# Optimization experiments

Measured on AMD Instinct MI355X. Metric: run time of the kernel, lower is better.

## Reference

```python
import jax, jax.numpy as jnp
import numpy as np

HEADS = 8
DIM_HEAD = 64
NUM_LANDMARKS = 256
PINV_ITERS = 6
SCALE = DIM_HEAD ** -0.5
KERNEL = 33
PAD = KERNEL // 2


def moore_penrose_iter_pinv(x, iters=PINV_ITERS):
    # x: [b, h, m, m]
    abs_x = jnp.abs(x)
    col = abs_x.sum(axis=-1)
    row = abs_x.sum(axis=-2)
    # global max over all batch/head entries, as in the torch code
    z = jnp.swapaxes(x, -1, -2) / (jnp.max(col) * jnp.max(row))
    I = jnp.eye(x.shape[-1], dtype=x.dtype)
    for _ in range(iters):
        xz = x @ z
        z = 0.25 * z @ (13.0 * I - xz @ (15.0 * I - xz @ (7.0 * I - xz)))
    return z


def setup_inputs() -> dict:
    key = jax.random.key(0)
    k1, k2, k3, k4 = jax.random.split(key, 4)
    b, n, dim = 4, 4096, 512
    inner = HEADS * DIM_HEAD
    return {
        "x": jax.random.normal(k1, (b, n, dim), dtype=jnp.float32),
        "w_qkv": jax.random.normal(k2, (dim, 3 * inner), dtype=jnp.float32) * 0.02,
        "w_out": jax.random.normal(k3, (inner, dim), dtype=jnp.float32) * 0.02,
        "b_out": jnp.zeros((dim,), dtype=jnp.float32),
        "conv_w": jax.random.normal(k4, (HEADS, 1, KERNEL, 1), dtype=jnp.float32) * 0.1,
    }


def reference(x, w_qkv, w_out, b_out, conv_w):
    b, n, dim = x.shape
    h, m = HEADS, NUM_LANDMARKS
    # n is a multiple of m, so the original's left-padding branch is a no-op
    qkv = x @ w_qkv  # [b, n, 3*h*d]
    q, k, v = jnp.split(qkv, 3, axis=-1)

    def split_heads(t):
        return t.reshape(b, n, h, DIM_HEAD).transpose(0, 2, 1, 3)  # [b,h,n,d]

    q, k, v = split_heads(q), split_heads(k), split_heads(v)
    q = q * SCALE

    l = n // m  # landmark group size
    q_l = q.reshape(b, h, m, l, DIM_HEAD).mean(axis=3)  # [b,h,m,d]
    k_l = k.reshape(b, h, m, l, DIM_HEAD).mean(axis=3)

    sim1 = jnp.einsum("bhid,bhjd->bhij", q, k_l)   # [b,h,n,m]
    sim2 = jnp.einsum("bhid,bhjd->bhij", q_l, k_l)  # [b,h,m,m]
    sim3 = jnp.einsum("bhid,bhjd->bhij", q_l, k)   # [b,h,m,n]

    attn1 = jax.nn.softmax(sim1, axis=-1)
    attn2 = jax.nn.softmax(sim2, axis=-1)
    attn3 = jax.nn.softmax(sim3, axis=-1)

    attn2_inv = moore_penrose_iter_pinv(attn2, PINV_ITERS)
    out = attn1 @ (attn2_inv @ (attn3 @ v))  # [b,h,n,d]

    # residual depthwise conv along sequence dim (kernel 33x1, groups=heads)
    res = jax.lax.conv_general_dilated(
        v, conv_w,
        window_strides=(1, 1),
        padding=((PAD, PAD), (0, 0)),
        dimension_numbers=("NCHW", "OIHW", "NCHW"),
        feature_group_count=h,
    )
    out = out + res

    out = out.transpose(0, 2, 1, 3).reshape(b, n, h * DIM_HEAD)
    out = out @ w_out + b_out
    return out  # out[:, -n:] is identity since no padding was applied
```

## Files before the change

kernel.cpp:

```cpp
#include <hip/hip_runtime.h>
#include <math.h>


#define QKV_STRIDE 262144
#define LM_STRIDE 16384
#define MM_STRIDE 65536

typedef float f32x4 __attribute__((ext_vector_type(4)));
typedef short bf8 __attribute__((ext_vector_type(8)));
typedef short s4v __attribute__((ext_vector_type(4)));

__device__ __forceinline__ unsigned short f2bf_(float f) {
  unsigned u = __float_as_uint(f);
  u += 0x7FFFu + ((u >> 16) & 1u);
  return (unsigned short)(u >> 16);
}
__device__ __forceinline__ float bf2f_(unsigned short h) {
  return __uint_as_float(((unsigned)h) << 16);
}
__device__ __forceinline__ bf8 pack8(const float4 a, const float4 b) {
  bf8 r;
  r[0] = (short)f2bf_(a.x); r[1] = (short)f2bf_(a.y);
  r[2] = (short)f2bf_(a.z); r[3] = (short)f2bf_(a.w);
  r[4] = (short)f2bf_(b.x); r[5] = (short)f2bf_(b.y);
  r[6] = (short)f2bf_(b.z); r[7] = (short)f2bf_(b.w);
  return r;
}

__global__ __launch_bounds__(256) void zero_scal(float* scal) {
  if (threadIdx.x < 2) scal[threadIdx.x] = 0.0f;
}

__global__ __launch_bounds__(256) void transpose_bf16(const float* __restrict__ src,
                                                      short* __restrict__ dst,
                                                      int R, int C) {
  __shared__ float T[32][33];
  const int t = threadIdx.x;
  const int c0 = blockIdx.x * 32, r0 = blockIdx.y * 32;
  const int tr = t >> 3, tc = (t & 7) << 2;
  float4 vsrc = *(const float4*)&src[(size_t)(r0 + tr) * C + c0 + tc];
  T[tr][tc + 0] = vsrc.x; T[tr][tc + 1] = vsrc.y;
  T[tr][tc + 2] = vsrc.z; T[tr][tc + 3] = vsrc.w;
  __syncthreads();
  s4v o;
  o[0] = (short)f2bf_(T[tc + 0][tr]);
  o[1] = (short)f2bf_(T[tc + 1][tr]);
  o[2] = (short)f2bf_(T[tc + 2][tr]);
  o[3] = (short)f2bf_(T[tc + 3][tr]);
  *(s4v*)&dst[(size_t)(c0 + tr) * R + r0 + tc] = o;
}

__global__ __launch_bounds__(256) void gemm_qkv_mfma(const float* __restrict__ x,
                                                     const short* __restrict__ wT,
                                                     short* __restrict__ qb16,
                                                     short* __restrict__ kb16,
                                                     short* __restrict__ vT16) {
  __shared__ short SMEM[17408];
  short* As = SMEM;
  short* Bs = SMEM + 4096;
  const int tid = threadIdx.x;
  const int lane = tid & 63, w = tid >> 6;
  const int wr = w >> 1, wc = w & 1;
  const int bid = (blockIdx.x & 7) * 192 + (blockIdx.x >> 3);
  const int bn = bid % 12, bm = bid / 12;
  const int gm0 = bm * 128, gn0 = bn * 128;
  const int mA0 = (tid >> 6) * 16 + (tid & 15), kA0 = ((tid >> 4) & 3) * 8;
  const int s1 = tid + 256;
  const int mA1 = (s1 >> 6) * 16 + (s1 & 15), kA1 = ((s1 >> 4) & 3) * 8;
  f32x4 acc[4][4];
#pragma unroll
  for (int i = 0; i < 4; ++i)
#pragma unroll
    for (int j = 0; j < 4; ++j) acc[i][j] = (f32x4){0.f, 0.f, 0.f, 0.f};
  for (int kt = 0; kt < 16; ++kt) {
    const int k0 = kt * 32;
    float4 a0 = *(const float4*)&x[(size_t)(gm0 + mA0) * 512 + k0 + kA0];
    float4 a1 = *(const float4*)&x[(size_t)(gm0 + mA0) * 512 + k0 + kA0 + 4];
    float4 a2 = *(const float4*)&x[(size_t)(gm0 + mA1) * 512 + k0 + kA1];
    float4 a3 = *(const float4*)&x[(size_t)(gm0 + mA1) * 512 + k0 + kA1 + 4];
    bf8 b0 = *(const bf8*)&wT[(size_t)(gn0 + mA0) * 512 + k0 + kA0];
    bf8 b1 = *(const bf8*)&wT[(size_t)(gn0 + mA1) * 512 + k0 + kA1];
    __syncthreads();
    *(bf8*)&As[tid * 8] = pack8(a0, a1);
    *(bf8*)&As[s1 * 8] = pack8(a2, a3);
    *(bf8*)&Bs[tid * 8] = b0;
    *(bf8*)&Bs[s1 * 8] = b1;
    __syncthreads();
    bf8 af[4], bf[4];
#pragma unroll
    for (int i = 0; i < 4; ++i) {
      af[i] = *(const bf8*)&As[((wr * 4 + i) * 64 + lane) * 8];
      bf[i] = *(const bf8*)&Bs[((wc * 4 + i) * 64 + lane) * 8];
    }
#pragma unroll
    for (int i = 0; i < 4; ++i)
#pragma unroll
      for (int j = 0; j < 4; ++j)
        acc[i][j] = __builtin_amdgcn_mfma_f32_16x16x32_bf16(af[i], bf[j], acc[i][j], 0, 0, 0);
  }
  const int which = bn >> 2;
  const int qd = lane >> 4, c = lane & 15;
  if (which < 2) {
    short* dst = which == 0 ? qb16 : kb16;
    const float scale = which == 0 ? 0.125f : 1.0f;
#pragma unroll
    for (int i = 0; i < 4; ++i)
#pragma unroll
      for (int j = 0; j < 4; ++j) {
        const int col = gn0 + wc * 64 + j * 16 + c;
        const int head = (col >> 6) & 7, dd = col & 63;
#pragma unroll
        for (int r = 0; r < 4; ++r) {
          const int row = gm0 + wr * 64 + i * 16 + qd * 4 + r;
          const int b = row >> 12, seq = row & 4095;
          dst[(size_t)(b * 8 + head) * QKV_STRIDE + seq * 64 + dd] =
              (short)f2bf_(acc[i][j][r] * scale);
        }
      }
  } else {
    __syncthreads();
#pragma unroll
    for (int i = 0; i < 4; ++i)
#pragma unroll
      for (int j = 0; j < 4; ++j) {
        const int colL = wc * 64 + j * 16 + c;
#pragma unroll
        for (int r = 0; r < 4; ++r) {
          const int rowL = wr * 64 + i * 16 + qd * 4 + r;
          SMEM[colL * 136 + rowL] = (short)f2bf_(acc[i][j][r]);
        }
      }
    __syncthreads();
    const int b = gm0 >> 12, seq0 = gm0 & 4095;
    const int dcol = tid >> 1, half = tid & 1;
    const int col = gn0 + dcol;
    const int head = (col >> 6) & 7, d = col & 63;
    const short* src = &SMEM[dcol * 136 + half * 64];
    short* dstp = &vT16[(size_t)(b * 8 + head) * QKV_STRIDE + (size_t)d * 4096 +
                        seq0 + half * 64];
#pragma unroll
    for (int u = 0; u < 16; ++u) *(s4v*)&dstp[u * 4] = *(const s4v*)&src[u * 4];
  }
}

__global__ __launch_bounds__(256) void lmk_mean(const short* __restrict__ qb16,
                                                const short* __restrict__ kb16,
                                                float* __restrict__ ql,
                                                float* __restrict__ kl,
                                                short* __restrict__ klb16) {
  const int g = blockIdx.x * 256 + threadIdx.x;
  const int dd = g & 63, mi = (g >> 6) & 255, bh = g >> 14;
  const size_t base = (size_t)bh * QKV_STRIDE + mi * 1024 + dd;
  float sq = 0.f, sk = 0.f;
#pragma unroll
  for (int jj = 0; jj < 16; ++jj) {
    sq += bf2f_((unsigned short)qb16[base + jj * 64]);
    sk += bf2f_((unsigned short)kb16[base + jj * 64]);
  }
  const float qv = sq * 0.0625f, kv = sk * 0.0625f;
  ql[g] = qv;
  kl[g] = kv;
  klb16[g] = (short)f2bf_(kv);
}

__global__ __launch_bounds__(256) void sim2_softmax(const float* __restrict__ ql,
                                                    const float* __restrict__ kl,
                                                    float* __restrict__ x2) {
  const int blk = blockIdx.x;
  const int bh = blk >> 4, rg = blk & 15;
  __shared__ float Qs[16][64];
  __shared__ float Ks[64][68];
  __shared__ float S[16][257];
  __shared__ float red[16][17];
  __shared__ float rowinv[16];
  const int tid = threadIdx.x;
  const int r = tid >> 4, jc = tid & 15;
#pragma unroll
  for (int u = 0; u < 4; ++u) {
    int t2 = tid + u * 256;
    Qs[t2 >> 6][t2 & 63] =
        ql[(size_t)bh * LM_STRIDE + (rg * 16 + (t2 >> 6)) * 64 + (t2 & 63)];
  }
  for (int c = 0; c < 4; ++c) {
    __syncthreads();
#pragma unroll
    for (int u = 0; u < 4; ++u) {
      int t4 = tid + u * 256;
      int row = t4 >> 4, c4 = (t4 & 15) << 2;
      *(float4*)&Ks[row][c4] =
          *(const float4*)&kl[(size_t)bh * LM_STRIDE + (c * 64 + row) * 64 + c4];
    }
    __syncthreads();
#pragma unroll
    for (int s = 0; s < 4; ++s) {
      const int jj = jc + (s << 4);
      float acc = 0.f;
#pragma unroll
      for (int k4 = 0; k4 < 16; ++k4) {
        const float4 a = *(const float4*)&Qs[r][k4 << 2];
        const float4 bb = *(const float4*)&Ks[jj][k4 << 2];
        acc += a.x * bb.x + a.y * bb.y + a.z * bb.z + a.w * bb.w;
      }
      S[r][(c << 6) + jj] = acc;
    }
  }
  __syncthreads();
  float pm = -3.0e38f;
#pragma unroll
  for (int u = 0; u < 16; ++u) pm = fmaxf(pm, S[r][jc + (u << 4)]);
  red[r][jc] = pm;
  __syncthreads();
  float m = red[r][0];
#pragma unroll
  for (int u = 1; u < 16; ++u) m = fmaxf(m, red[r][u]);
  __syncthreads();
  float ps = 0.f;
#pragma unroll
  for (int u = 0; u < 16; ++u) {
    const int j = jc + (u << 4);
    const float e = __expf(S[r][j] - m);
    S[r][j] = e;
    ps += e;
  }
  red[r][jc] = ps;
  __syncthreads();
  if (jc == 0) {
    float sum = 0.f;
#pragma unroll
    for (int u = 0; u < 16; ++u) sum += red[r][u];
    rowinv[r] = 1.0f / sum;
  }
  __syncthreads();
  for (int idx = tid; idx < 4096; idx += 256) {
    const int rr = idx >> 8, j = idx & 255;
    x2[(size_t)bh * MM_STRIDE + (rg * 16 + rr) * 256 + j] = S[rr][j] * rowinv[rr];
  }
}

__global__ __launch_bounds__(256) void colrow_max(const float* __restrict__ x2,
                                                  float* __restrict__ scal) {
  const int bh = blockIdx.x;
  const int tid = threadIdx.x;
  const float* xb = x2 + (size_t)bh * MM_STRIDE;
  float cs = 0.f, rs = 0.f;
  for (int j = 0; j < 256; ++j) cs += fabsf(xb[tid * 256 + j]);
  for (int i = 0; i < 256; ++i) rs += fabsf(xb[i * 256 + tid]);
  __shared__ float rc[256], rr[256];
  rc[tid] = cs; rr[tid] = rs;
  __syncthreads();
  for (int st = 128; st > 0; st >>= 1) {
    if (tid < st) {
      rc[tid] = fmaxf(rc[tid], rc[tid + st]);
      rr[tid] = fmaxf(rr[tid], rr[tid + st]);
    }
    __syncthreads();
  }
  if (tid == 0) {
    atomicMax((int*)&scal[0], __float_as_int(rc[0]));
    atomicMax((int*)&scal[1], __float_as_int(rr[0]));
  }
}

__global__ __launch_bounds__(256) void tscale2(const float* __restrict__ x2,
                                               const float* __restrict__ scal,
                                               float* __restrict__ z0,
                                               float* __restrict__ z0t) {
  const int g = blockIdx.x * 256 + threadIdx.x;
  const int j = g & 255, i = (g >> 8) & 255, bh = g >> 16;
  const float inv = 1.0f / (scal[0] * scal[1]);
  const float val = x2[g] * inv;
  z0t[g] = val;
  z0[(size_t)bh * MM_STRIDE + j * 256 + i] = val;
}

__global__ __launch_bounds__(256) void pinv_mfma(const float* __restrict__ A,
                                                 const float* __restrict__ BT,
                                                 const float* __restrict__ E,
                                                 float* __restrict__ C,
                                                 float* __restrict__ CT,
                                                 float alpha, float beta,
                                                 int wantC, int wantT) {
  __shared__ short Ahi[2048], Alo[2048], Bhi[2048], Blo[2048];
  __shared__ float Tbuf[64 * 68];
  const int tid = threadIdx.x;
  const int lane = tid & 63, w = tid >> 6;
  const int bid = blockIdx.x;
  const int xcd = bid & 7, y = bid >> 3;
  const int t16 = y & 15, bgrp = y >> 4;
  const int batch = bgrp * 8 + xcd;
  const int tm = t16 >> 2, tn = t16 & 3;
  const float* Ab = A + (size_t)batch * MM_STRIDE;
  const float* BTb = BT + (size_t)batch * MM_STRIDE;
  const float* Eb = E + (size_t)batch * MM_STRIDE;
  const int ml = (tid >> 6) * 16 + (tid & 15), koff = ((tid >> 4) & 3) * 8;
  f32x4 acc[4];
#pragma unroll
  for (int j = 0; j < 4; ++j) acc[j] = (f32x4){0.f, 0.f, 0.f, 0.f};
  for (int kt = 0; kt < 8; ++kt) {
    const int k0 = kt * 32;
    float4 a0 = *(const float4*)&Ab[(size_t)(tm * 64 + ml) * 256 + k0 + koff];
    float4 a1 = *(const float4*)&Ab[(size_t)(tm * 64 + ml) * 256 + k0 + koff + 4];
    float4 b0 = *(const float4*)&BTb[(size_t)(tn * 64 + ml) * 256 + k0 + koff];
    float4 b1 = *(const float4*)&BTb[(size_t)(tn * 64 + ml) * 256 + k0 + koff + 4];
    __syncthreads();
    {
      bf8 hi, lo;
      const float fa[8] = {a0.x, a0.y, a0.z, a0.w, a1.x, a1.y, a1.z, a1.w};
#pragma unroll
      for (int e = 0; e < 8; ++e) {
        unsigned short h = f2bf_(fa[e]);
        hi[e] = (short)h;
        lo[e] = (short)f2bf_(fa[e] - bf2f_(h));
      }
      *(bf8*)&Ahi[tid * 8] = hi;
      *(bf8*)&Alo[tid * 8] = lo;
      const float fb[8] = {b0.x, b0.y, b0.z, b0.w, b1.x, b1.y, b1.z, b1.w};
#pragma unroll
      for (int e = 0; e < 8; ++e) {
        unsigned short h = f2bf_(fb[e]);
        hi[e] = (short)h;
        lo[e] = (short)f2bf_(fb[e] - bf2f_(h));
      }
      *(bf8*)&Bhi[tid * 8] = hi;
      *(bf8*)&Blo[tid * 8] = lo;
    }
    __syncthreads();
    bf8 ah = *(const bf8*)&Ahi[(w * 64 + lane) * 8];
    bf8 al = *(const bf8*)&Alo[(w * 64 + lane) * 8];
#pragma unroll
    for (int j = 0; j < 4; ++j) {
      bf8 bh = *(const bf8*)&Bhi[(j * 64 + lane) * 8];
      bf8 bl = *(const bf8*)&Blo[(j * 64 + lane) * 8];
      acc[j] = __builtin_amdgcn_mfma_f32_16x16x32_bf16(ah, bh, acc[j], 0, 0, 0);
      acc[j] = __builtin_amdgcn_mfma_f32_16x16x32_bf16(ah, bl, acc[j], 0, 0, 0);
      acc[j] = __builtin_amdgcn_mfma_f32_16x16x32_bf16(al, bh, acc[j], 0, 0, 0);
    }
  }
  float* Cb = C + (size_t)batch * MM_STRIDE;
  float* CTb = CT + (size_t)batch * MM_STRIDE;
  const int qd = lane >> 4, c = lane & 15;
  float vals[4][4];
#pragma unroll
  for (int j = 0; j < 4; ++j) {
    const int col = tn * 64 + j * 16 + c;
#pragma unroll
    for (int r = 0; r < 4; ++r) {
      const int row = tm * 64 + w * 16 + qd * 4 + r;
      vals[j][r] = alpha * Eb[(size_t)row * 256 + col] + beta * acc[j][r];
      if (wantC) Cb[(size_t)row * 256 + col] = vals[j][r];
    }
  }
  if (wantT) {
    __syncthreads();
#pragma unroll
    for (int j = 0; j < 4; ++j)
#pragma unroll
      for (int r = 0; r < 4; ++r)
        Tbuf[(j * 16 + c) * 68 + w * 16 + qd * 4 + r] = vals[j][r];
    __syncthreads();
    const int ctr = tid >> 2, seg = (tid & 3) * 16;
#pragma unroll
    for (int u = 0; u < 4; ++u) {
      float4 o = *(const float4*)&Tbuf[ctr * 68 + seg + u * 4];
      *(float4*)&CTb[(size_t)(tn * 64 + ctr) * 256 + tm * 64 + seg + u * 4] = o;
    }
  }
}

__global__ __launch_bounds__(256) void attn3_flash(const float* __restrict__ ql,
                                                   const short* __restrict__ kb16,
                                                   const short* __restrict__ vT16,
                                                   float* __restrict__ opart,
                                                   float* __restrict__ mpart,
                                                   float* __restrict__ lpart) {
  const int kc = blockIdx.x;
  const int rt = blockIdx.y;
  const int bh = blockIdx.z;
  __shared__ short Pa[4][4096];
  const int tid = threadIdx.x, lane = tid & 63, w = tid >> 6;
  const int qd = lane >> 4, c = lane & 15;
  const int rw = rt * 64 + w * 16;
  const float* qlp = ql + (size_t)bh * LM_STRIDE;
  const short* kp = kb16 + (size_t)bh * QKV_STRIDE;
  const short* vp = vT16 + (size_t)bh * QKV_STRIDE;
  short* Pw = &Pa[w][0];
  bf8 af[2];
#pragma unroll
  for (int st = 0; st < 2; ++st) {
    float4 x0 = *(const float4*)&qlp[(size_t)(rw + c) * 64 + st * 32 + qd * 8];
    float4 x1 = *(const float4*)&qlp[(size_t)(rw + c) * 64 + st * 32 + qd * 8 + 4];
    af[st] = pack8(x0, x1);
  }
  float m[4], l[4];
#pragma unroll
  for (int r = 0; r < 4; ++r) { m[r] = -3.0e38f; l[r] = 0.f; }
  f32x4 accO[4];
#pragma unroll
  for (int nb = 0; nb < 4; ++nb) accO[nb] = (f32x4){0.f, 0.f, 0.f, 0.f};
  for (int it = 0; it < 4; ++it) {
    const int kb0 = kc * 1024 + it * 256;
    f32x4 acc[16];
#pragma unroll
    for (int j = 0; j < 16; ++j) acc[j] = (f32x4){0.f, 0.f, 0.f, 0.f};
#pragma unroll
    for (int st = 0; st < 2; ++st)
#pragma unroll
      for (int j = 0; j < 16; ++j) {
        bf8 bfk = *(const bf8*)&kp[(size_t)(kb0 + j * 16 + c) * 64 + st * 32 + qd * 8];
        acc[j] = __builtin_amdgcn_mfma_f32_16x16x32_bf16(af[st], bfk, acc[j], 0, 0, 0);
      }
#pragma unroll
    for (int r = 0; r < 4; ++r) {
      float mx = acc[0][r];
#pragma unroll
      for (int j = 1; j < 16; ++j) mx = fmaxf(mx, acc[j][r]);
      mx = fmaxf(mx, __shfl_xor(mx, 1));
      mx = fmaxf(mx, __shfl_xor(mx, 2));
      mx = fmaxf(mx, __shfl_xor(mx, 4));
      mx = fmaxf(mx, __shfl_xor(mx, 8));
      const float mN = fmaxf(m[r], mx);
      const float a = __expf(m[r] - mN);
      m[r] = mN;
      l[r] *= a;
#pragma unroll
      for (int nb = 0; nb < 4; ++nb) accO[nb][r] *= a;
      float s = 0.f;
#pragma unroll
      for (int j = 0; j < 16; ++j) {
        const float e = __expf(acc[j][r] - mN);
        acc[j][r] = e;
        s += e;
      }
      s += __shfl_xor(s, 1);
      s += __shfl_xor(s, 2);
      s += __shfl_xor(s, 4);
      s += __shfl_xor(s, 8);
      l[r] += s;
    }
#pragma unroll
    for (int j = 0; j < 16; ++j) {
      const int kcol = j * 16 + c;
      const int kb8 = kcol >> 5;
      const int la_base = 16 * ((kcol >> 3) & 3);
      const int j8 = kcol & 7;
#pragma unroll
      for (int r = 0; r < 4; ++r) {
        const int rl = qd * 4 + r;
        Pw[(kb8 * 64 + la_base + rl) * 8 + j8] = (short)f2bf_(acc[j][r]);
      }
    }
#pragma unroll
    for (int kbk = 0; kbk < 8; ++kbk) {
      bf8 ap = *(const bf8*)&Pw[(kbk * 64 + lane) * 8];
#pragma unroll
      for (int nb = 0; nb < 4; ++nb) {
        bf8 bv = *(const bf8*)&vp[(size_t)(nb * 16 + c) * 4096 + kb0 + kbk * 32 + qd * 8];
        accO[nb] = __builtin_amdgcn_mfma_f32_16x16x32_bf16(ap, bv, accO[nb], 0, 0, 0);
      }
    }
  }
  const size_t ob = ((size_t)kc * 32 + bh) * 256 + rt * 64;
#pragma unroll
  for (int nb = 0; nb < 4; ++nb)
#pragma unroll
    for (int r = 0; r < 4; ++r)
      opart[(ob + w * 16 + qd * 4 + r) * 64 + nb * 16 + c] = accO[nb][r];
  if (c == 0) {
#pragma unroll
    for (int r = 0; r < 4; ++r) {
      mpart[ob + w * 16 + qd * 4 + r] = m[r];
      lpart[ob + w * 16 + qd * 4 + r] = l[r];
    }
  }
}

__global__ __launch_bounds__(256) void attn3_merge(const float* __restrict__ opart,
                                                   const float* __restrict__ mpart,
                                                   const float* __restrict__ lpart,
                                                   short* __restrict__ avth,
                                                   short* __restrict__ avtl) {
  const int g = blockIdx.x * 256 + threadIdx.x;
  const int d = g & 63;
  const int idx = g >> 6;
  const int bh = idx >> 8, row = idx & 255;
  const float m0 = mpart[idx], m1 = mpart[8192 + idx],
              m2 = mpart[16384 + idx], m3 = mpart[24576 + idx];
  const float mx = fmaxf(fmaxf(m0, m1), fmaxf(m2, m3));
  const float w0 = __expf(m0 - mx), w1 = __expf(m1 - mx),
              w2 = __expf(m2 - mx), w3 = __expf(m3 - mx);
  const float l = lpart[idx] * w0 + lpart[8192 + idx] * w1 +
                  lpart[16384 + idx] * w2 + lpart[24576 + idx] * w3;
  const float o = opart[(size_t)idx * 64 + d] * w0 +
                  opart[524288 + (size_t)idx * 64 + d] * w1 +
                  opart[1048576 + (size_t)idx * 64 + d] * w2 +
                  opart[1572864 + (size_t)idx * 64 + d] * w3;
  const float val = o / l;
  const unsigned short h = f2bf_(val);
  const size_t o2 = ((size_t)bh * 64 + d) * 256 + row;
  avth[o2] = (short)h;
  avtl[o2] = (short)f2bf_(val - bf2f_(h));
}

__global__ __launch_bounds__(256) void zav_mfma(const float* __restrict__ z,
                                                const short* __restrict__ avth,
                                                const short* __restrict__ avtl,
                                                short* __restrict__ w2tb16) {
  __shared__ short Tb[64 * 68];
  const int rt = blockIdx.x;
  const int bh = blockIdx.y;
  const int tid = threadIdx.x, lane = tid & 63, w = tid >> 6;
  const int qd = lane >> 4, c = lane & 15;
  const float* zp = z + (size_t)bh * MM_STRIDE + (size_t)(rt * 64 + w * 16 + c) * 256;
  const short* ahp = avth + (size_t)bh * LM_STRIDE;
  const short* alp = avtl + (size_t)bh * LM_STRIDE;
  f32x4 acc[4];
#pragma unroll
  for (int j = 0; j < 4; ++j) acc[j] = (f32x4){0.f, 0.f, 0.f, 0.f};
  for (int kt = 0; kt < 8; ++kt) {
    const int k0 = kt * 32 + qd * 8;
    float4 a0 = *(const float4*)&zp[k0];
    float4 a1 = *(const float4*)&zp[k0 + 4];
    bf8 ah, al;
    const float fa[8] = {a0.x, a0.y, a0.z, a0.w, a1.x, a1.y, a1.z, a1.w};
#pragma unroll
    for (int e = 0; e < 8; ++e) {
      const unsigned short h = f2bf_(fa[e]);
      ah[e] = (short)h;
      al[e] = (short)f2bf_(fa[e] - bf2f_(h));
    }
#pragma unroll
    for (int j = 0; j < 4; ++j) {
      bf8 bhj = *(const bf8*)&ahp[(size_t)(j * 16 + c) * 256 + k0];
      bf8 blj = *(const bf8*)&alp[(size_t)(j * 16 + c) * 256 + k0];
      acc[j] = __builtin_amdgcn_mfma_f32_16x16x32_bf16(ah, bhj, acc[j], 0, 0, 0);
      acc[j] = __builtin_amdgcn_mfma_f32_16x16x32_bf16(ah, blj, acc[j], 0, 0, 0);
      acc[j] = __builtin_amdgcn_mfma_f32_16x16x32_bf16(al, bhj, acc[j], 0, 0, 0);
    }
  }
#pragma unroll
  for (int j = 0; j < 4; ++j)
#pragma unroll
    for (int r = 0; r < 4; ++r)
      Tb[(j * 16 + c) * 68 + w * 16 + qd * 4 + r] = (short)f2bf_(acc[j][r]);
  __syncthreads();
  const int col = tid >> 2, rs = (tid & 3) * 16;
  short* dst = &w2tb16[(size_t)bh * LM_STRIDE + (size_t)col * 256 + rt * 64 + rs];
  const short* srcp = &Tb[col * 68 + rs];
#pragma unroll
  for (int u = 0; u < 4; ++u) *(s4v*)&dst[u * 4] = *(const s4v*)&srcp[u * 4];
}

__global__ __launch_bounds__(256) void attn1_conv_mfma(const short* __restrict__ qb16,
                                                       const short* __restrict__ klb16,
                                                       const short* __restrict__ w2tb16,
                                                       const short* __restrict__ vT16,
                                                       const float* __restrict__ cw,
                                                       short* __restrict__ ohb16) {
  __shared__ short Pa[16384];
  __shared__ float redM[4][64], redS[4][64];
  __shared__ float rowM[64], rowI[64];
  __shared__ float cwS[33];
  const int tid = threadIdx.x;
  const int lane = tid & 63, w = tid >> 6;
  const int qd = lane >> 4, c = lane & 15;
  const int r0 = blockIdx.x * 64;
  const int bh = blockIdx.y;
  const short* qp = qb16 + (size_t)bh * QKV_STRIDE;
  const short* klp = klb16 + (size_t)bh * LM_STRIDE;
  const short* w2p = w2tb16 + (size_t)bh * LM_STRIDE;
  const short* vp = vT16 + (size_t)bh * QKV_STRIDE;

  if (tid < 33) cwS[tid] = cw[(bh & 7) * 33 + tid];

  f32x4 acc[4][4];
#pragma unroll
  for (int i = 0; i < 4; ++i)
#pragma unroll
    for (int j = 0; j < 4; ++j) acc[i][j] = (f32x4){0.f, 0.f, 0.f, 0.f};
#pragma unroll
  for (int st = 0; st < 2; ++st) {
    const int k0 = st * 32 + qd * 8;
    bf8 af[4], bf[4];
#pragma unroll
    for (int i = 0; i < 4; ++i) {
      af[i] = *(const bf8*)&qp[(size_t)(r0 + i * 16 + c) * 64 + k0];
      bf[i] = *(const bf8*)&klp[(size_t)(w * 64 + i * 16 + c) * 64 + k0];
    }
#pragma unroll
    for (int i = 0; i < 4; ++i)
#pragma unroll
      for (int j = 0; j < 4; ++j)
        acc[i][j] = __builtin_amdgcn_mfma_f32_16x16x32_bf16(af[i], bf[j], acc[i][j], 0, 0, 0);
  }
#pragma unroll
  for (int i = 0; i < 4; ++i)
#pragma unroll
    for (int r = 0; r < 4; ++r) {
      float m0 = fmaxf(fmaxf(acc[i][0][r], acc[i][1][r]),
                       fmaxf(acc[i][2][r], acc[i][3][r]));
      m0 = fmaxf(m0, __shfl_xor(m0, 1));
      m0 = fmaxf(m0, __shfl_xor(m0, 2));
      m0 = fmaxf(m0, __shfl_xor(m0, 4));
      m0 = fmaxf(m0, __shfl_xor(m0, 8));
      if (c == 0) redM[w][i * 16 + qd * 4 + r] = m0;
    }
  __syncthreads();
  if (tid < 64)
    rowM[tid] = fmaxf(fmaxf(redM[0][tid], redM[1][tid]),
                      fmaxf(redM[2][tid], redM[3][tid]));
  __syncthreads();
#pragma unroll
  for (int i = 0; i < 4; ++i)
#pragma unroll
    for (int r = 0; r < 4; ++r) {
      const float mrow = rowM[i * 16 + qd * 4 + r];
      float s = 0.f;
#pragma unroll
      for (int j = 0; j < 4; ++j) {
        const float e = __expf(acc[i][j][r] - mrow);
        acc[i][j][r] = e;
        s += e;
      }
      s += __shfl_xor(s, 1);
      s += __shfl_xor(s, 2);
      s += __shfl_xor(s, 4);
      s += __shfl_xor(s, 8);
      if (c == 0) redS[w][i * 16 + qd * 4 + r] = s;
    }
  __syncthreads();
  if (tid < 64)
    rowI[tid] = 1.0f / (redS[0][tid] + redS[1][tid] + redS[2][tid] + redS[3][tid]);
  __syncthreads();
#pragma unroll
  for (int i = 0; i < 4; ++i)
#pragma unroll
    for (int r = 0; r < 4; ++r) {
      const int row = i * 16 + qd * 4 + r;
      const float inv = rowI[row];
#pragma unroll
      for (int j = 0; j < 4; ++j) {
        const int col = w * 64 + j * 16 + c;
        const short val = (short)f2bf_(acc[i][j][r] * inv);
        const int kb = col >> 5;
        const int lane2 = (row & 15) + 16 * ((col >> 3) & 3);
        Pa[((kb * 4 + i) * 64 + lane2) * 8 + (col & 7)] = val;
      }
    }
  __syncthreads();
  f32x4 accO[4];
#pragma unroll
  for (int nb = 0; nb < 4; ++nb) accO[nb] = (f32x4){0.f, 0.f, 0.f, 0.f};
  for (int kb = 0; kb < 8; ++kb) {
    bf8 ap = *(const bf8*)&Pa[((kb * 4 + w) * 64 + lane) * 8];
#pragma unroll
    for (int nb = 0; nb < 4; ++nb) {
      bf8 bfr = *(const bf8*)&w2p[(size_t)(nb * 16 + c) * 256 + kb * 32 + qd * 8];
      accO[nb] = __builtin_amdgcn_mfma_f32_16x16x32_bf16(ap, bfr, accO[nb], 0, 0, 0);
    }
  }
  {
    bf8 ba[3];
    const int rl = w * 16 + (lane & 15);
#pragma unroll
    for (int kb = 0; kb < 3; ++kb) {
#pragma unroll
      for (int e = 0; e < 8; ++e) {
        const int kk = kb * 32 + qd * 8 + e;
        const int t = kk - rl;
        const int s = r0 - 16 + kk;
        const float bv = (t >= 0 && t < 33 && s >= 0 && s < 4096) ? cwS[t] : 0.f;
        ba[kb][e] = (short)f2bf_(bv);
      }
    }
#pragma unroll
    for (int kb = 0; kb < 3; ++kb) {
      int s0 = r0 - 16 + kb * 32 + qd * 8;
      s0 = s0 < 0 ? 0 : (s0 > 4088 ? 4088 : s0);
#pragma unroll
      for (int nb = 0; nb < 4; ++nb) {
        bf8 bv = *(const bf8*)&vp[(size_t)(nb * 16 + c) * 4096 + s0];
        accO[nb] = __builtin_amdgcn_mfma_f32_16x16x32_bf16(ba[kb], bv, accO[nb], 0, 0, 0);
      }
    }
  }
  short* ohp = (short*)ohb16 + (size_t)bh * QKV_STRIDE;
#pragma unroll
  for (int nb = 0; nb < 4; ++nb)
#pragma unroll
    for (int r = 0; r < 4; ++r) {
      const int row = r0 + w * 16 + qd * 4 + r;
      ohp[(size_t)row * 64 + nb * 16 + c] = (short)f2bf_(accO[nb][r]);
    }
}

__global__ __launch_bounds__(256) void gemm_out_mfma(const short* __restrict__ ohb16,
                                                     const short* __restrict__ wT,
                                                     const float* __restrict__ bias,
                                                     float* __restrict__ out) {
  __shared__ short As[4096];
  __shared__ short Bs[4096];
  const int tid = threadIdx.x;
  const int lane = tid & 63, w = tid >> 6;
  const int wr = w >> 1, wc = w & 1;
  const int bid = (blockIdx.x & 7) * 64 + (blockIdx.x >> 3);
  const int bn = bid & 3, bm = bid >> 2;
  const int gm0 = bm * 128, gn0 = bn * 128;
  const int mA0 = (tid >> 6) * 16 + (tid & 15), kA0 = ((tid >> 4) & 3) * 8;
  const int s1 = tid + 256;
  const int mA1 = (s1 >> 6) * 16 + (s1 & 15), kA1 = ((s1 >> 4) & 3) * 8;
  const int b0r = (gm0 + mA0) >> 12, seq0 = (gm0 + mA0) & 4095;
  const int b1r = (gm0 + mA1) >> 12, seq1 = (gm0 + mA1) & 4095;
  f32x4 acc[4][4];
#pragma unroll
  for (int i = 0; i < 4; ++i)
#pragma unroll
    for (int j = 0; j < 4; ++j) acc[i][j] = (f32x4){0.f, 0.f, 0.f, 0.f};
  for (int kt = 0; kt < 16; ++kt) {
    const int k0 = kt * 32;
    const int ka = k0 + kA0, kb = k0 + kA1;
    bf8 aa0 = *(const bf8*)&ohb16[(size_t)(b0r * 8 + (ka >> 6)) * QKV_STRIDE + seq0 * 64 + (ka & 63)];
    bf8 aa1 = *(const bf8*)&ohb16[(size_t)(b1r * 8 + (kb >> 6)) * QKV_STRIDE + seq1 * 64 + (kb & 63)];
    bf8 bb0 = *(const bf8*)&wT[(size_t)(gn0 + mA0) * 512 + ka];
    bf8 bb1 = *(const bf8*)&wT[(size_t)(gn0 + mA1) * 512 + kb];
    __syncthreads();
    *(bf8*)&As[tid * 8] = aa0;
    *(bf8*)&As[s1 * 8] = aa1;
    *(bf8*)&Bs[tid * 8] = bb0;
    *(bf8*)&Bs[s1 * 8] = bb1;
    __syncthreads();
    bf8 af[4], bfr[4];
#pragma unroll
    for (int i = 0; i < 4; ++i) {
      af[i] = *(const bf8*)&As[((wr * 4 + i) * 64 + lane) * 8];
      bfr[i] = *(const bf8*)&Bs[((wc * 4 + i) * 64 + lane) * 8];
    }
#pragma unroll
    for (int i = 0; i < 4; ++i)
#pragma unroll
      for (int j = 0; j < 4; ++j)
        acc[i][j] = __builtin_amdgcn_mfma_f32_16x16x32_bf16(af[i], bfr[j], acc[i][j], 0, 0, 0);
  }
  const int qd = lane >> 4, c = lane & 15;
#pragma unroll
  for (int i = 0; i < 4; ++i)
#pragma unroll
    for (int j = 0; j < 4; ++j) {
      const int col = gn0 + wc * 64 + j * 16 + c;
      const float bval = bias[col];
#pragma unroll
      for (int r = 0; r < 4; ++r) {
        const int row = gm0 + wr * 64 + i * 16 + qd * 4 + r;
        out[(size_t)row * 512 + col] = acc[i][j][r] + bval;
      }
    }
}

extern "C" void kernel_launch(void* const* d_in, const int* in_sizes, int n_in,
                              void* d_out, int out_size, void* d_ws, size_t ws_size,
                              hipStream_t stream) {
  const float* x    = (const float*)d_in[0];
  const float* wqkv = (const float*)d_in[1];
  const float* wout = (const float*)d_in[2];
  const float* bout = (const float*)d_in[3];
  const float* cw   = (const float*)d_in[4];
  float* out = (float*)d_out;

  float* w = (float*)d_ws;
  short* qb16   = (short*)(w);
  short* kb16   = (short*)(w + 4194304);
  short* vT16   = (short*)(w + 8388608);
  short* ohb16  = (short*)(w + 12582912);
  float* ql     = w + 16777216;
  float* kl     = w + 17301504;
  short* klb16  = (short*)(w + 17825792);
  float* x2     = w + 18087936;
  float* z0     = w + 20185088;
  float* z0t    = w + 22282240;
  float* z1     = w + 24379392;
  float* z1t    = w + 26476544;
  float* xz     = w + 28573696;
  float* xzt    = w + 30670848;
  float* u1t    = w + 32768000;
  float* u2t    = w + 34865152;
  short* avth   = (short*)(w + 36962304);
  short* avtl   = (short*)(w + 37224448);
  short* w2tb16 = (short*)(w + 37486592);
  float* scal   = w + 37748736;
  short* wqkvT  = (short*)(w + 37748800);
  short* woutT  = (short*)(w + 38142016);
  float* opart = z1;
  float* mpart = z1t;
  float* lpart = z1t + 32768;

  zero_scal<<<1, 64, 0, stream>>>(scal);
  transpose_bf16<<<dim3(48, 16), 256, 0, stream>>>(wqkv, wqkvT, 512, 1536);
  transpose_bf16<<<dim3(16, 16), 256, 0, stream>>>(wout, woutT, 512, 512);
  gemm_qkv_mfma<<<1536, 256, 0, stream>>>(x, wqkvT, qb16, kb16, vT16);
  lmk_mean<<<2048, 256, 0, stream>>>(qb16, kb16, ql, kl, klb16);
  sim2_softmax<<<512, 256, 0, stream>>>(ql, kl, x2);
  colrow_max<<<32, 256, 0, stream>>>(x2, scal);
  tscale2<<<8192, 256, 0, stream>>>(x2, scal, z0, z0t);

  float *zc = z0, *zct = z0t, *zn = z1, *znt = z1t;
  for (int it = 0; it < 6; ++it) {
    pinv_mfma<<<512, 256, 0, stream>>>(x2, zct, x2, xz, xzt, 0.f, 1.f, 1, 1);
    pinv_mfma<<<512, 256, 0, stream>>>(xz, xzt, xz, u1t, u1t, 7.f, -1.f, 0, 1);
    pinv_mfma<<<512, 256, 0, stream>>>(xz, u1t, xz, u2t, u2t, 15.f, -1.f, 0, 1);
    pinv_mfma<<<512, 256, 0, stream>>>(zc, u2t, zc, zn, znt, 3.25f, -0.25f, 1, 1);
    float* t;
    t = zc; zc = zn; zn = t;
    t = zct; zct = znt; znt = t;
  }

  attn3_flash<<<dim3(4, 4, 32), 256, 0, stream>>>(ql, kb16, vT16, opart, mpart, lpart);
  attn3_merge<<<2048, 256, 0, stream>>>(opart, mpart, lpart, avth, avtl);
  zav_mfma<<<dim3(4, 32), 256, 0, stream>>>(zc, avth, avtl, w2tb16);
  attn1_conv_mfma<<<dim3(64, 32), 256, 0, stream>>>(qb16, klb16, w2tb16, vT16, cw, ohb16);
  gemm_out_mfma<<<512, 256, 0, stream>>>(ohb16, woutT, bout, out);
}
```

Before: 820.7 us.

## Use direct global-to-LDS loads and pre-split bf16 hi/lo operands in pinv chain

The GEMM kernels now load tiles with global_load_lds (16-byte direct-to-LDS) instead of staging through registers. The input x is converted to bf16 in a separate pass so the QKV GEMM can use direct loads. The Newton-Schulz pinv chain now stores its intermediates as precomputed bf16 hi/lo pairs rather than fp32, so each GEMM skips the per-tile split and reads half the bytes per operand copy. The cost is an extra conversion kernel, more split work in the epilogues, and a reorganised workspace layout that aliases several buffers.

```diff
diff --git a/kernel.cpp b/kernel.cpp
--- a/kernel.cpp
+++ b/kernel.cpp
@@ -18,17 +18,30 @@
 __device__ __forceinline__ float bf2f_(unsigned short h) {
   return __uint_as_float(((unsigned)h) << 16);
 }
-__device__ __forceinline__ bf8 pack8(const float4 a, const float4 b) {
-  bf8 r;
-  r[0] = (short)f2bf_(a.x); r[1] = (short)f2bf_(a.y);
-  r[2] = (short)f2bf_(a.z); r[3] = (short)f2bf_(a.w);
-  r[4] = (short)f2bf_(b.x); r[5] = (short)f2bf_(b.y);
-  r[6] = (short)f2bf_(b.z); r[7] = (short)f2bf_(b.w);
-  return r;
+
+__device__ __forceinline__ void gl16(const short* g, short* l) {
+  __builtin_amdgcn_global_load_lds(
+      (const __attribute__((address_space(1))) unsigned int*)g,
+      (__attribute__((address_space(3))) unsigned int*)l, 16, 0, 0);
 }
 
 __global__ __launch_bounds__(256) void zero_scal(float* scal) {
   if (threadIdx.x < 2) scal[threadIdx.x] = 0.0f;
+}
+
+__global__ __launch_bounds__(256) void x_to_bf16(const float* __restrict__ x,
+                                                 short* __restrict__ xb) {
+  const int g = blockIdx.x * 256 + threadIdx.x;
+  const float4* xp = (const float4*)x;
+#pragma unroll
+  for (int u = 0; u < 4; ++u) {
+    const size_t i4 = (size_t)u * 524288 + g;
+    float4 v = xp[i4];
+    s4v o;
+    o[0] = (short)f2bf_(v.x); o[1] = (short)f2bf_(v.y);
+    o[2] = (short)f2bf_(v.z); o[3] = (short)f2bf_(v.w);
+    *(s4v*)&xb[i4 * 4] = o;
+  }
 }
 
 __global__ __launch_bounds__(256) void transpose_bf16(const float* __restrict__ src,
@@ -50,7 +63,7 @@
   *(s4v*)&dst[(size_t)(c0 + tr) * R + r0 + tc] = o;
 }
 
-__global__ __launch_bounds__(256) void gemm_qkv_mfma(const float* __restrict__ x,
+__global__ __launch_bounds__(256) void gemm_qkv_mfma(const short* __restrict__ xb,
                                                      const short* __restrict__ wT,
                                                      short* __restrict__ qb16,
                                                      short* __restrict__ kb16,
@@ -67,6 +80,14 @@
   const int mA0 = (tid >> 6) * 16 + (tid & 15), kA0 = ((tid >> 4) & 3) * 8;
   const int s1 = tid + 256;
   const int mA1 = (s1 >> 6) * 16 + (s1 & 15), kA1 = ((s1 >> 4) & 3) * 8;
+  const short* srcA0 = &xb[(size_t)(gm0 + mA0) * 512 + kA0];
+  const short* srcA1 = &xb[(size_t)(gm0 + mA1) * 512 + kA1];
+  const short* srcB0 = &wT[(size_t)(gn0 + mA0) * 512 + kA0];
+  const short* srcB1 = &wT[(size_t)(gn0 + mA1) * 512 + kA1];
+  short* dA0 = &As[w * 512];
+  short* dA1 = &As[2048 + w * 512];
+  short* dB0 = &Bs[w * 512];
+  short* dB1 = &Bs[2048 + w * 512];
   f32x4 acc[4][4];
 #pragma unroll
   for (int i = 0; i < 4; ++i)
@@ -74,17 +95,11 @@
     for (int j = 0; j < 4; ++j) acc[i][j] = (f32x4){0.f, 0.f, 0.f, 0.f};
   for (int kt = 0; kt < 16; ++kt) {
     const int k0 = kt * 32;
-    float4 a0 = *(const float4*)&x[(size_t)(gm0 + mA0) * 512 + k0 + kA0];
-    float4 a1 = *(const float4*)&x[(size_t)(gm0 + mA0) * 512 + k0 + kA0 + 4];
-    float4 a2 = *(const float4*)&x[(size_t)(gm0 + mA1) * 512 + k0 + kA1];
-    float4 a3 = *(const float4*)&x[(size_t)(gm0 + mA1) * 512 + k0 + kA1 + 4];
-    bf8 b0 = *(const bf8*)&wT[(size_t)(gn0 + mA0) * 512 + k0 + kA0];
-    bf8 b1 = *(const bf8*)&wT[(size_t)(gn0 + mA1) * 512 + k0 + kA1];
-    __syncthreads();
-    *(bf8*)&As[tid * 8] = pack8(a0, a1);
-    *(bf8*)&As[s1 * 8] = pack8(a2, a3);
-    *(bf8*)&Bs[tid * 8] = b0;
-    *(bf8*)&Bs[s1 * 8] = b1;
+    __syncthreads();
+    gl16(srcA0 + k0, dA0);
+    gl16(srcA1 + k0, dA1);
+    gl16(srcB0 + k0, dB0);
+    gl16(srcB1 + k0, dB1);
     __syncthreads();
     bf8 af[4], bf[4];
 #pragma unroll
@@ -165,7 +180,8 @@
 
 __global__ __launch_bounds__(256) void sim2_softmax(const float* __restrict__ ql,
                                                     const float* __restrict__ kl,
-                                                    float* __restrict__ x2) {
+                                                    short* __restrict__ x2hi,
+                                                    short* __restrict__ x2lo) {
   const int blk = blockIdx.x;
   const int bh = blk >> 4, rg = blk & 15;
   __shared__ float Qs[16][64];
@@ -233,18 +249,29 @@
   __syncthreads();
   for (int idx = tid; idx < 4096; idx += 256) {
     const int rr = idx >> 8, j = idx & 255;
-    x2[(size_t)bh * MM_STRIDE + (rg * 16 + rr) * 256 + j] = S[rr][j] * rowinv[rr];
-  }
-}
-
-__global__ __launch_bounds__(256) void colrow_max(const float* __restrict__ x2,
+    const float v = S[rr][j] * rowinv[rr];
+    const unsigned short h = f2bf_(v);
+    const size_t off = (size_t)bh * MM_STRIDE + (rg * 16 + rr) * 256 + j;
+    x2hi[off] = (short)h;
+    x2lo[off] = (short)f2bf_(v - bf2f_(h));
+  }
+}
+
+__global__ __launch_bounds__(256) void colrow_max(const short* __restrict__ x2hi,
+                                                  const short* __restrict__ x2lo,
                                                   float* __restrict__ scal) {
   const int bh = blockIdx.x;
   const int tid = threadIdx.x;
-  const float* xb = x2 + (size_t)bh * MM_STRIDE;
+  const size_t b0 = (size_t)bh * MM_STRIDE;
   float cs = 0.f, rs = 0.f;
-  for (int j = 0; j < 256; ++j) cs += fabsf(xb[tid * 256 + j]);
-  for (int i = 0; i < 256; ++i) rs += fabsf(xb[i * 256 + tid]);
+  for (int j = 0; j < 256; ++j) {
+    const size_t o = b0 + (size_t)tid * 256 + j;
+    cs += fabsf(bf2f_((unsigned short)x2hi[o]) + bf2f_((unsigned short)x2lo[o]));
+  }
+  for (int i = 0; i < 256; ++i) {
+    const size_t o = b0 + (size_t)i * 256 + tid;
+    rs += fabsf(bf2f_((unsigned short)x2hi[o]) + bf2f_((unsigned short)x2lo[o]));
+  }
   __shared__ float rc[256], rr[256];
   rc[tid] = cs; rr[tid] = rs;
   __syncthreads();
@@ -261,26 +288,43 @@
   }
 }
 
-__global__ __launch_bounds__(256) void tscale2(const float* __restrict__ x2,
+__global__ __launch_bounds__(256) void tscale2(const short* __restrict__ x2hi,
+                                               const short* __restrict__ x2lo,
                                                const float* __restrict__ scal,
-                                               float* __restrict__ z0,
-                                               float* __restrict__ z0t) {
+                                               short* __restrict__ zBhi,
+                                               short* __restrict__ zBlo,
+                                               short* __restrict__ zAhi,
+                                               short* __restrict__ zAlo,
+                                               float* __restrict__ zf) {
   const int g = blockIdx.x * 256 + threadIdx.x;
   const int j = g & 255, i = (g >> 8) & 255, bh = g >> 16;
   const float inv = 1.0f / (scal[0] * scal[1]);
-  const float val = x2[g] * inv;
-  z0t[g] = val;
-  z0[(size_t)bh * MM_STRIDE + j * 256 + i] = val;
-}
-
-__global__ __launch_bounds__(256) void pinv_mfma(const float* __restrict__ A,
-                                                 const float* __restrict__ BT,
-                                                 const float* __restrict__ E,
-                                                 float* __restrict__ C,
-                                                 float* __restrict__ CT,
+  const float val = (bf2f_((unsigned short)x2hi[g]) +
+                     bf2f_((unsigned short)x2lo[g])) * inv;
+  const unsigned short h = f2bf_(val);
+  const unsigned short lo = f2bf_(val - bf2f_(h));
+  zBhi[g] = (short)h;
+  zBlo[g] = (short)lo;
+  const size_t tg = (size_t)bh * MM_STRIDE + (size_t)j * 256 + i;
+  zAhi[tg] = (short)h;
+  zAlo[tg] = (short)lo;
+  zf[tg] = val;
+}
+
+__global__ __launch_bounds__(256) void pinv_mfma(const short* __restrict__ Ahi_g,
+                                                 const short* __restrict__ Alo_g,
+                                                 const short* __restrict__ Bhi_g,
+                                                 const short* __restrict__ Blo_g,
+                                                 const float* __restrict__ Ef,
+                                                 float* __restrict__ Cf,
+                                                 short* __restrict__ Chi,
+                                                 short* __restrict__ Clo,
+                                                 short* __restrict__ CThi,
+                                                 short* __restrict__ CTlo,
                                                  float alpha, float beta,
-                                                 int wantC, int wantT) {
-  __shared__ short Ahi[2048], Alo[2048], Bhi[2048], Blo[2048];
+                                                 int wantCf, int wantChl,
+                                                 int wantT) {
+  __shared__ short Ah[2048], Al[2048], Bh[2048], Bl[2048];
   __shared__ float Tbuf[64 * 68];
   const int tid = threadIdx.x;
   const int lane = tid & 63, w = tid >> 6;
@@ -289,55 +333,38 @@
   const int t16 = y & 15, bgrp = y >> 4;
   const int batch = bgrp * 8 + xcd;
   const int tm = t16 >> 2, tn = t16 & 3;
-  const float* Ab = A + (size_t)batch * MM_STRIDE;
-  const float* BTb = BT + (size_t)batch * MM_STRIDE;
-  const float* Eb = E + (size_t)batch * MM_STRIDE;
+  const size_t bb = (size_t)batch * MM_STRIDE;
   const int ml = (tid >> 6) * 16 + (tid & 15), koff = ((tid >> 4) & 3) * 8;
+  const short* sAh = Ahi_g + bb + (size_t)(tm * 64 + ml) * 256 + koff;
+  const short* sAl = Alo_g + bb + (size_t)(tm * 64 + ml) * 256 + koff;
+  const short* sBh = Bhi_g + bb + (size_t)(tn * 64 + ml) * 256 + koff;
+  const short* sBl = Blo_g + bb + (size_t)(tn * 64 + ml) * 256 + koff;
+  short* dAh = &Ah[w * 512];
+  short* dAl = &Al[w * 512];
+  short* dBh = &Bh[w * 512];
+  short* dBl = &Bl[w * 512];
   f32x4 acc[4];
 #pragma unroll
   for (int j = 0; j < 4; ++j) acc[j] = (f32x4){0.f, 0.f, 0.f, 0.f};
   for (int kt = 0; kt < 8; ++kt) {
     const int k0 = kt * 32;
-    float4 a0 = *(const float4*)&Ab[(size_t)(tm * 64 + ml) * 256 + k0 + koff];
-    float4 a1 = *(const float4*)&Ab[(size_t)(tm * 64 + ml) * 256 + k0 + koff + 4];
-    float4 b0 = *(const float4*)&BTb[(size_t)(tn * 64 + ml) * 256 + k0 + koff];
-    float4 b1 = *(const float4*)&BTb[(size_t)(tn * 64 + ml) * 256 + k0 + koff + 4];
-    __syncthreads();
-    {
-      bf8 hi, lo;
-      const float fa[8] = {a0.x, a0.y, a0.z, a0.w, a1.x, a1.y, a1.z, a1.w};
-#pragma unroll
-      for (int e = 0; e < 8; ++e) {
-        unsigned short h = f2bf_(fa[e]);
-        hi[e] = (short)h;
-        lo[e] = (short)f2bf_(fa[e] - bf2f_(h));
-      }
-      *(bf8*)&Ahi[tid * 8] = hi;
-      *(bf8*)&Alo[tid * 8] = lo;
-      const float fb[8] = {b0.x, b0.y, b0.z, b0.w, b1.x, b1.y, b1.z, b1.w};
-#pragma unroll
-      for (int e = 0; e < 8; ++e) {
-        unsigned short h = f2bf_(fb[e]);
-        hi[e] = (short)h;
-        lo[e] = (short)f2bf_(fb[e] - bf2f_(h));
-      }
-      *(bf8*)&Bhi[tid * 8] = hi;
-      *(bf8*)&Blo[tid * 8] = lo;
-    }
-    __syncthreads();
-    bf8 ah = *(const bf8*)&Ahi[(w * 64 + lane) * 8];
-    bf8 al = *(const bf8*)&Alo[(w * 64 + lane) * 8];
+    __syncthreads();
+    gl16(sAh + k0, dAh);
+    gl16(sAl + k0, dAl);
+    gl16(sBh + k0, dBh);
+    gl16(sBl + k0, dBl);
+    __syncthreads();
+    bf8 ah = *(const bf8*)&Ah[(w * 64 + lane) * 8];
+    bf8 al = *(const bf8*)&Al[(w * 64 + lane) * 8];
 #pragma unroll
     for (int j = 0; j < 4; ++j) {
-      bf8 bh = *(const bf8*)&Bhi[(j * 64 + lane) * 8];
-      bf8 bl = *(const bf8*)&Blo[(j * 64 + lane) * 8];
+      bf8 bh = *(const bf8*)&Bh[(j * 64 + lane) * 8];
+      bf8 bl = *(const bf8*)&Bl[(j * 64 + lane) * 8];
       acc[j] = __builtin_amdgcn_mfma_f32_16x16x32_bf16(ah, bh, acc[j], 0, 0, 0);
       acc[j] = __builtin_amdgcn_mfma_f32_16x16x32_bf16(ah, bl, acc[j], 0, 0, 0);
       acc[j] = __builtin_amdgcn_mfma_f32_16x16x32_bf16(al, bh, acc[j], 0, 0, 0);
     }
   }
-  float* Cb = C + (size_t)batch * MM_STRIDE;
-  float* CTb = CT + (size_t)batch * MM_STRIDE;
   const int qd = lane >> 4, c = lane & 15;
   float vals[4][4];
 #pragma unroll
@@ -346,8 +373,17 @@
 #pragma unroll
     for (int r = 0; r < 4; ++r) {
       const int row = tm * 64 + w * 16 + qd * 4 + r;
-      vals[j][r] = alpha * Eb[(size_t)row * 256 + col] + beta * acc[j][r];
-      if (wantC) Cb[(size_t)row * 256 + col] = vals[j][r];
+      const size_t off = bb + (size_t)row * 256 + col;
+      float e = 0.f;
+      if (alpha != 0.0f) e = alpha * Ef[off];
+      const float vv = e + beta * acc[j][r];
+      vals[j][r] = vv;
+      if (wantCf) Cf[off] = vv;
+      if (wantChl) {
+        const unsigned short h = f2bf_(vv);
+        Chi[off] = (short)h;
+        Clo[off] = (short)f2bf_(vv - bf2f_(h));
+      }
     }
   }
   if (wantT) {
@@ -362,7 +398,15 @@
 #pragma unroll
     for (int u = 0; u < 4; ++u) {
       float4 o = *(const float4*)&Tbuf[ctr * 68 + seg + u * 4];
-      *(float4*)&CTb[(size_t)(tn * 64 + ctr) * 256 + tm * 64 + seg + u * 4] = o;
+      s4v hi, lo;
+      unsigned short h;
+      h = f2bf_(o.x); hi[0] = (short)h; lo[0] = (short)f2bf_(o.x - bf2f_(h));
+      h = f2bf_(o.y); hi[1] = (short)h; lo[1] = (short)f2bf_(o.y - bf2f_(h));
+      h = f2bf_(o.z); hi[2] = (short)h; lo[2] = (short)f2bf_(o.z - bf2f_(h));
+      h = f2bf_(o.w); hi[3] = (short)h; lo[3] = (short)f2bf_(o.w - bf2f_(h));
+      const size_t off = bb + (size_t)(tn * 64 + ctr) * 256 + tm * 64 + seg + u * 4;
+      *(s4v*)&CThi[off] = hi;
+      *(s4v*)&CTlo[off] = lo;
     }
   }
 }
@@ -389,7 +433,12 @@
   for (int st = 0; st < 2; ++st) {
     float4 x0 = *(const float4*)&qlp[(size_t)(rw + c) * 64 + st * 32 + qd * 8];
     float4 x1 = *(const float4*)&qlp[(size_t)(rw + c) * 64 + st * 32 + qd * 8 + 4];
-    af[st] = pack8(x0, x1);
+    bf8 r;
+    r[0] = (short)f2bf_(x0.x); r[1] = (short)f2bf_(x0.y);
+    r[2] = (short)f2bf_(x0.z); r[3] = (short)f2bf_(x0.w);
+    r[4] = (short)f2bf_(x1.x); r[5] = (short)f2bf_(x1.y);
+    r[6] = (short)f2bf_(x1.z); r[7] = (short)f2bf_(x1.w);
+    af[st] = r;
   }
   float m[4], l[4];
 #pragma unroll
@@ -501,7 +550,8 @@
   avtl[o2] = (short)f2bf_(val - bf2f_(h));
 }
 
-__global__ __launch_bounds__(256) void zav_mfma(const float* __restrict__ z,
+__global__ __launch_bounds__(256) void zav_mfma(const short* __restrict__ zAhi,
+                                                const short* __restrict__ zAlo,
                                                 const short* __restrict__ avth,
                                                 const short* __restrict__ avtl,
                                                 short* __restrict__ w2tb16) {
@@ -510,7 +560,9 @@
   const int bh = blockIdx.y;
   const int tid = threadIdx.x, lane = tid & 63, w = tid >> 6;
   const int qd = lane >> 4, c = lane & 15;
-  const float* zp = z + (size_t)bh * MM_STRIDE + (size_t)(rt * 64 + w * 16 + c) * 256;
+  const size_t zoff = (size_t)bh * MM_STRIDE + (size_t)(rt * 64 + w * 16 + c) * 256;
+  const short* zh = zAhi + zoff;
+  const short* zl = zAlo + zoff;
   const short* ahp = avth + (size_t)bh * LM_STRIDE;
   const short* alp = avtl + (size_t)bh * LM_STRIDE;
   f32x4 acc[4];
@@ -518,16 +570,8 @@
   for (int j = 0; j < 4; ++j) acc[j] = (f32x4){0.f, 0.f, 0.f, 0.f};
   for (int kt = 0; kt < 8; ++kt) {
     const int k0 = kt * 32 + qd * 8;
-    float4 a0 = *(const float4*)&zp[k0];
-    float4 a1 = *(const float4*)&zp[k0 + 4];
-    bf8 ah, al;
-    const float fa[8] = {a0.x, a0.y, a0.z, a0.w, a1.x, a1.y, a1.z, a1.w};
-#pragma unroll
-    for (int e = 0; e < 8; ++e) {
-      const unsigned short h = f2bf_(fa[e]);
-      ah[e] = (short)h;
-      al[e] = (short)f2bf_(fa[e] - bf2f_(h));
-    }
+    bf8 ah = *(const bf8*)&zh[k0];
+    bf8 al = *(const bf8*)&zl[k0];
 #pragma unroll
     for (int j = 0; j < 4; ++j) {
       bf8 bhj = *(const bf8*)&ahp[(size_t)(j * 16 + c) * 256 + k0];
@@ -710,23 +754,22 @@
   const int mA1 = (s1 >> 6) * 16 + (s1 & 15), kA1 = ((s1 >> 4) & 3) * 8;
   const int b0r = (gm0 + mA0) >> 12, seq0 = (gm0 + mA0) & 4095;
   const int b1r = (gm0 + mA1) >> 12, seq1 = (gm0 + mA1) & 4095;
+  short* dA0 = &As[w * 512];
+  short* dA1 = &As[2048 + w * 512];
+  short* dB0 = &Bs[w * 512];
+  short* dB1 = &Bs[2048 + w * 512];
   f32x4 acc[4][4];
 #pragma unroll
   for (int i = 0; i < 4; ++i)
 #pragma unroll
     for (int j = 0; j < 4; ++j) acc[i][j] = (f32x4){0.f, 0.f, 0.f, 0.f};
   for (int kt = 0; kt < 16; ++kt) {
-    const int k0 = kt * 32;
-    const int ka = k0 + kA0, kb = k0 + kA1;
-    bf8 aa0 = *(const bf8*)&ohb16[(size_t)(b0r * 8 + (ka >> 6)) * QKV_STRIDE + seq0 * 64 + (ka & 63)];
-    bf8 aa1 = *(const bf8*)&ohb16[(size_t)(b1r * 8 + (kb >> 6)) * QKV_STRIDE + seq1 * 64 + (kb & 63)];
-    bf8 bb0 = *(const bf8*)&wT[(size_t)(gn0 + mA0) * 512 + ka];
-    bf8 bb1 = *(const bf8*)&wT[(size_t)(gn0 + mA1) * 512 + kb];
-    __syncthreads();
-    *(bf8*)&As[tid * 8] = aa0;
-    *(bf8*)&As[s1 * 8] = aa1;
-    *(bf8*)&Bs[tid * 8] = bb0;
-    *(bf8*)&Bs[s1 * 8] = bb1;
+    const int ka = kt * 32 + kA0, kb = kt * 32 + kA1;
+    __syncthreads();
+    gl16(&ohb16[(size_t)(b0r * 8 + (ka >> 6)) * QKV_STRIDE + (size_t)seq0 * 64 + (ka & 63)], dA0);
+    gl16(&ohb16[(size_t)(b1r * 8 + (kb >> 6)) * QKV_STRIDE + (size_t)seq1 * 64 + (kb & 63)], dA1);
+    gl16(&wT[(size_t)(gn0 + mA0) * 512 + ka], dB0);
+    gl16(&wT[(size_t)(gn0 + mA1) * 512 + kb], dB1);
     __syncthreads();
     bf8 af[4], bfr[4];
 #pragma unroll
@@ -769,52 +812,75 @@
   short* qb16   = (short*)(w);
   short* kb16   = (short*)(w + 4194304);
   short* vT16   = (short*)(w + 8388608);
+  short* xb16   = (short*)(w + 12582912);
+  float* z0f    = w + 12582912;
+  float* z1f    = w + 14680064;
+  float* opart  = w + 12582912;
   short* ohb16  = (short*)(w + 12582912);
   float* ql     = w + 16777216;
   float* kl     = w + 17301504;
   short* klb16  = (short*)(w + 17825792);
-  float* x2     = w + 18087936;
-  float* z0     = w + 20185088;
-  float* z0t    = w + 22282240;
-  float* z1     = w + 24379392;
-  float* z1t    = w + 26476544;
-  float* xz     = w + 28573696;
-  float* xzt    = w + 30670848;
-  float* u1t    = w + 32768000;
-  float* u2t    = w + 34865152;
-  short* avth   = (short*)(w + 36962304);
-  short* avtl   = (short*)(w + 37224448);
-  short* w2tb16 = (short*)(w + 37486592);
-  float* scal   = w + 37748736;
-  short* wqkvT  = (short*)(w + 37748800);
-  short* woutT  = (short*)(w + 38142016);
-  float* opart = z1;
-  float* mpart = z1t;
-  float* lpart = z1t + 32768;
+  short* x2hi   = (short*)(w + 18087936);
+  short* x2lo   = (short*)(w + 19136512);
+  float* xzf    = w + 20185088;
+  short* xzAhi  = (short*)(w + 22282240);
+  short* xzAlo  = (short*)(w + 23330816);
+  short* xzBhi  = (short*)(w + 24379392);
+  short* xzBlo  = (short*)(w + 25427968);
+  short* u1Bhi  = (short*)(w + 26476544);
+  short* u1Blo  = (short*)(w + 27525120);
+  short* z0Ahi  = (short*)(w + 28573696);
+  short* z0Alo  = (short*)(w + 29622272);
+  short* z0Bhi  = (short*)(w + 30670848);
+  short* z0Blo  = (short*)(w + 31719424);
+  short* z1Ahi  = (short*)(w + 32768000);
+  short* z1Alo  = (short*)(w + 33816576);
+  short* z1Bhi  = (short*)(w + 34865152);
+  short* z1Blo  = (short*)(w + 35913728);
+  float* scal   = w + 36962304;
+  short* wqkvT  = (short*)(w + 36962368);
+  short* woutT  = (short*)(w + 37355584);
+  short* avth   = (short*)(w + 20185088);
+  short* avtl   = (short*)(w + 20447232);
+  short* w2tb16 = (short*)(w + 20709376);
+  float* mpart  = w + 26476544;
+  float* lpart  = w + 26509312;
 
   zero_scal<<<1, 64, 0, stream>>>(scal);
   transpose_bf16<<<dim3(48, 16), 256, 0, stream>>>(wqkv, wqkvT, 512, 1536);
   transpose_bf16<<<dim3(16, 16), 256, 0, stream>>>(wout, woutT, 512, 512);
-  gemm_qkv_mfma<<<1536, 256, 0, stream>>>(x, wqkvT, qb16, kb16, vT16);
+  x_to_bf16<<<2048, 256, 0, stream>>>(x, xb16);
+  gemm_qkv_mfma<<<1536, 256, 0, stream>>>(xb16, wqkvT, qb16, kb16, vT16);
   lmk_mean<<<2048, 256, 0, stream>>>(qb16, kb16, ql, kl, klb16);
-  sim2_softmax<<<512, 256, 0, stream>>>(ql, kl, x2);
-  colrow_max<<<32, 256, 0, stream>>>(x2, scal);
-  tscale2<<<8192, 256, 0, stream>>>(x2, scal, z0, z0t);
-
-  float *zc = z0, *zct = z0t, *zn = z1, *znt = z1t;
+  sim2_softmax<<<512, 256, 0, stream>>>(ql, kl, x2hi, x2lo);
+  colrow_max<<<32, 256, 0, stream>>>(x2hi, x2lo, scal);
+  tscale2<<<8192, 256, 0, stream>>>(x2hi, x2lo, scal, z0Bhi, z0Blo, z0Ahi, z0Alo, z0f);
+
+  float *zcf = z0f, *znf = z1f;
+  short *zAh = z0Ahi, *zAl = z0Alo, *zBh = z0Bhi, *zBl = z0Blo;
+  short *nAh = z1Ahi, *nAl = z1Alo, *nBh = z1Bhi, *nBl = z1Blo;
   for (int it = 0; it < 6; ++it) {
-    pinv_mfma<<<512, 256, 0, stream>>>(x2, zct, x2, xz, xzt, 0.f, 1.f, 1, 1);
-    pinv_mfma<<<512, 256, 0, stream>>>(xz, xzt, xz, u1t, u1t, 7.f, -1.f, 0, 1);
-    pinv_mfma<<<512, 256, 0, stream>>>(xz, u1t, xz, u2t, u2t, 15.f, -1.f, 0, 1);
-    pinv_mfma<<<512, 256, 0, stream>>>(zc, u2t, zc, zn, znt, 3.25f, -0.25f, 1, 1);
-    float* t;
-    t = zc; zc = zn; zn = t;
-    t = zct; zct = znt; znt = t;
+    pinv_mfma<<<512, 256, 0, stream>>>(x2hi, x2lo, zBh, zBl, xzf,
+                                       xzf, xzAhi, xzAlo, xzBhi, xzBlo,
+                                       0.f, 1.f, 1, 1, 1);
+    pinv_mfma<<<512, 256, 0, stream>>>(xzAhi, xzAlo, xzBhi, xzBlo, xzf,
+                                       znf, u1Bhi, u1Blo, u1Bhi, u1Blo,
+                                       7.f, -1.f, 0, 0, 1);
+    pinv_mfma<<<512, 256, 0, stream>>>(xzAhi, xzAlo, u1Bhi, u1Blo, xzf,
+                                       znf, xzBhi, xzBlo, xzBhi, xzBlo,
+                                       15.f, -1.f, 0, 0, 1);
+    pinv_mfma<<<512, 256, 0, stream>>>(zAh, zAl, xzBhi, xzBlo, zcf,
+                                       znf, nAh, nAl, nBh, nBl,
+                                       3.25f, -0.25f, 1, 1, 1);
+    float* tf = zcf; zcf = znf; znf = tf;
+    short* t;
+    t = zAh; zAh = nAh; nAh = t;  t = zAl; zAl = nAl; nAl = t;
+    t = zBh; zBh = nBh; nBh = t;  t = zBl; zBl = nBl; nBl = t;
   }
 
   attn3_flash<<<dim3(4, 4, 32), 256, 0, stream>>>(ql, kb16, vT16, opart, mpart, lpart);
   attn3_merge<<<2048, 256, 0, stream>>>(opart, mpart, lpart, avth, avtl);
-  zav_mfma<<<dim3(4, 32), 256, 0, stream>>>(zc, avth, avtl, w2tb16);
+  zav_mfma<<<dim3(4, 32), 256, 0, stream>>>(zAh, zAl, avth, avtl, w2tb16);
   attn1_conv_mfma<<<dim3(64, 32), 256, 0, stream>>>(qb16, klb16, w2tb16, vT16, cw, ohb16);
   gemm_out_mfma<<<512, 256, 0, stream>>>(ohb16, woutT, bout, out);
 }
```

After: 801.4 us. 1.02x faster.
